# Performance work log

Hardware: AMD Instinct MI355X
Metric: run time of the kernel (lower is better)

## Reference

```python
import jax, jax.numpy as jnp
import numpy as np

B, T, D = 4, 2048, 2048
H, HD = 16, 128  # n_heads, head_dim; inner_dim = H*HD = 2048
SCALE = float(np.sqrt(HD))


def setup_inputs() -> dict:
    key = jax.random.key(0)
    kx, kq, kk, kv, ko = jax.random.split(key, 5)
    s = 0.02
    return {
        "x":  jax.random.normal(kx, (B, T, D), jnp.float32),
        "Wq": jax.random.normal(kq, (D, H * HD), jnp.float32) * s,
        "Wk": jax.random.normal(kk, (D, H * HD), jnp.float32) * s,
        "Wv": jax.random.normal(kv, (D, H * HD), jnp.float32) * s,
        "Wo": jax.random.normal(ko, (H * HD, D), jnp.float32) * s,
        "layer_idx": 0,
    }


def reference(x, Wq, Wk, Wv, Wo, layer_idx):
    # Cache starts empty and T <= max_cache_size, so cached_k/v == k/v and
    # T_cache == T; the sink/window mask reduces to a standard causal mask.
    b, t, _ = x.shape

    def split_heads(y):
        return y.reshape(b, t, H, HD).transpose(0, 2, 1, 3)  # (B,H,T,HD)

    q = split_heads(x @ Wq)
    k = split_heads(x @ Wk)
    v = split_heads(x @ Wv)

    scores = jnp.einsum('bhqd,bhkd->bhqk', q, k) / SCALE  # (B,H,T,T)
    q_idx = jnp.arange(t)
    k_idx = jnp.arange(t)
    causal = k_idx[None, :] <= q_idx[:, None]  # T_cache - T + q_idx == q_idx
    scores = jnp.where(causal[None, None], scores, -jnp.inf)
    w = jax.nn.softmax(scores, axis=-1)
    out = jnp.einsum('bhqk,bhkd->bhqd', w, v)
    out = out.transpose(0, 2, 1, 3).reshape(b, t, H * HD)
    return out @ Wo
```

## Files before the change

kernel.cpp:

```cpp
#include <hip/hip_runtime.h>
#include <hip/hip_bf16.h>
#include <stdint.h>

#define TT   2048
#define DD   2048
#define NH   16
#define NB   4
#define HDIM 128
#define MSZ  (NB * TT)
#define NQKV (3 * DD)
#define NT   32

typedef __attribute__((ext_vector_type(8))) __bf16 bf16x8;
typedef __attribute__((ext_vector_type(4))) float  f32x4;

typedef __attribute__((address_space(3))) void       lds_void;
typedef const __attribute__((address_space(1))) void g_void;

__device__ inline unsigned short f2bf(float f) {
  union { float f; unsigned u; } v; v.f = f;
  unsigned r = v.u + 0x7fffu + ((v.u >> 16) & 1u);
  return (unsigned short)(r >> 16);
}

__device__ inline void gload16(const void* g, void* l) {
  __builtin_amdgcn_global_load_lds((g_void*)g, (lds_void*)l, 16, 0, 0);
}

__device__ inline f32x4 mfma16(bf16x8 a, bf16x8 b, f32x4 c) {
  return __builtin_amdgcn_mfma_f32_16x16x32_bf16(a, b, c, 0, 0, 0);
}

__global__ __launch_bounds__(256) void cvtx(const float* __restrict__ x,
                                            unsigned short* __restrict__ xb) {
  const int n4 = MSZ * DD / 4;
  for (int i = blockIdx.x * blockDim.x + threadIdx.x; i < n4;
       i += gridDim.x * blockDim.x) {
    float4 v = ((const float4*)x)[i];
    uint2 u;
    u.x = (unsigned)f2bf(v.x) | ((unsigned)f2bf(v.y) << 16);
    u.y = (unsigned)f2bf(v.z) | ((unsigned)f2bf(v.w) << 16);
    *(uint2*)&xb[(size_t)i * 4] = u;
  }
}

__global__ __launch_bounds__(256) void transW(const float* __restrict__ Wq,
                                              const float* __restrict__ Wk,
                                              const float* __restrict__ Wv,
                                              const float* __restrict__ Wo,
                                              unsigned short* __restrict__ Wtq,
                                              unsigned short* __restrict__ Wto) {
  __shared__ float tl[32][33];
  const int z = blockIdx.z;
  const float* W = (z == 0) ? Wq : (z == 1) ? Wk : (z == 2) ? Wv : Wo;
  unsigned short* outp = (z < 3) ? (Wtq + (size_t)z * DD * DD) : Wto;
  const int c = threadIdx.x & 31, r8 = threadIdx.x >> 5;
  const int k0 = blockIdx.y * 32, n0 = blockIdx.x * 32;
#pragma unroll
  for (int i = 0; i < 4; ++i)
    tl[r8 + 8 * i][c] = W[(size_t)(k0 + r8 + 8 * i) * DD + n0 + c];
  __syncthreads();
#pragma unroll
  for (int i = 0; i < 4; ++i)
    outp[(size_t)(n0 + r8 + 8 * i) * DD + k0 + c] = f2bf(tl[c][r8 + 8 * i]);
}

template <int EPI>
__global__ __launch_bounds__(512, 2) void gemm8(
    const unsigned short* __restrict__ A, const unsigned short* __restrict__ Bt,
    unsigned short* __restrict__ Qb, unsigned short* __restrict__ Kb,
    unsigned short* __restrict__ Vt, float* __restrict__ Cf) {
  __shared__ __align__(16) unsigned short As[2][2][8192];
  __shared__ __align__(16) unsigned short Bs[2][2][8192];
  const int tid = threadIdx.x;
  const int lane = tid & 63;
  const int w = tid >> 6;
  const int wm = w >> 2, wn = w & 3;
  const int l15 = lane & 15, g = lane >> 4;
  const int m0 = blockIdx.y * 256, n0 = blockIdx.x * 256;

  const int u  = (tid * 16) ^ (((tid >> 5) & 1) << 5);
  const int sr = (u >> 6) & 127;
  const int sc = (u & 63) >> 1;
  const unsigned short* sA0 = A  + (size_t)(m0 + sr) * DD + sc;
  const unsigned short* sA1 = A  + (size_t)(m0 + 128 + sr) * DD + sc;
  const unsigned short* sB0 = Bt + (size_t)(n0 + sr) * DD + sc;
  const unsigned short* sB1 = Bt + (size_t)(n0 + 128 + sr) * DD + sc;

  const int pA = ((l15 * 64 + g * 16) ^ (((l15 >> 3) & 1) << 5)) >> 1;
  const int pB = (wn & 1) * 2048 + pA;

  f32x4 acc[8][4] = {};

#define STAGE(kt, hf)                                                         \
  do {                                                                        \
    if ((kt) < NT) {                                                          \
      const unsigned short* s_ = (hf) == 0 ? sA0 : (hf) == 1 ? sA1            \
                                 : (hf) == 2 ? sB0 : sB1;                     \
      s_ += (kt) * 64;                                                        \
      unsigned short* d_ = ((hf) < 2 ? &As[(kt) & 1][(hf) & 1][0]             \
                                     : &Bs[(kt) & 1][(hf) & 1][0]) + tid * 8; \
      gload16(s_, d_);                                                        \
      gload16(s_ + 32, d_ + 4096);                                            \
    }                                                                         \
  } while (0)

#define MFMAQ(q)                                                              \
  do {                                                                        \
    __builtin_amdgcn_s_setprio(1);                                            \
    _Pragma("unroll") for (int n2 = 0; n2 < 2; ++n2)                          \
    _Pragma("unroll") for (int m2 = 0; m2 < 4; ++m2)                          \
    _Pragma("unroll") for (int kk = 0; kk < 2; ++kk)                          \
      acc[((q) & 1) * 4 + m2][((q) >> 1) * 2 + n2] =                          \
          mfma16(af[((q) & 1) * 4 + m2][kk], bq[((q) >> 1) * 2 + n2][kk],     \
                 acc[((q) & 1) * 4 + m2][((q) >> 1) * 2 + n2]);               \
    __builtin_amdgcn_s_setprio(0);                                            \
  } while (0)

#define TILE(t, buf)                                                          \
  do {                                                                        \
    const unsigned short* Ab = &As[buf][wm][0];                               \
    const unsigned short* Bb = &Bs[buf][wn >> 1][0];                          \
    bf16x8 af[8][2], bq[4][2];                                                \
    _Pragma("unroll") for (int m = 0; m < 8; ++m) {                           \
      af[m][0] = *(const bf16x8*)&Ab[pA + m * 512];                           \
      af[m][1] = *(const bf16x8*)&Ab[pA + m * 512 + 4096];                    \
    }                                                                         \
    _Pragma("unroll") for (int n = 0; n < 4; ++n) {                           \
      bq[n][0] = *(const bf16x8*)&Bb[pB + n * 512];                           \
      bq[n][1] = *(const bf16x8*)&Bb[pB + n * 512 + 4096];                    \
    }                                                                         \
    STAGE((t) + 1, 3);                                                        \
    __builtin_amdgcn_s_barrier();                                             \
    MFMAQ(0);                                                                 \
    asm volatile("s_waitcnt lgkmcnt(0)" ::: "memory");                        \
    __builtin_amdgcn_sched_barrier(0);                                        \
    __builtin_amdgcn_s_barrier();                                             \
    STAGE((t) + 2, 0);                                                        \
    __builtin_amdgcn_s_barrier();                                             \
    MFMAQ(1);                                                                 \
    __builtin_amdgcn_s_barrier();                                             \
    STAGE((t) + 2, 1);                                                        \
    __builtin_amdgcn_s_barrier();                                             \
    MFMAQ(2);                                                                 \
    __builtin_amdgcn_s_barrier();                                             \
    STAGE((t) + 2, 2);                                                        \
    __builtin_amdgcn_s_barrier();                                             \
    MFMAQ(3);                                                                 \
    asm volatile("s_waitcnt vmcnt(6)" ::: "memory");                          \
    __builtin_amdgcn_sched_barrier(0);                                        \
    __builtin_amdgcn_s_barrier();                                             \
  } while (0)

  STAGE(0, 0); STAGE(0, 1); STAGE(0, 2); STAGE(0, 3);
  STAGE(1, 0); STAGE(1, 1); STAGE(1, 2);
  asm volatile("s_waitcnt vmcnt(6)" ::: "memory");
  __builtin_amdgcn_sched_barrier(0);
  __builtin_amdgcn_s_barrier();

#pragma unroll 1
  for (int it = 0; it < NT / 2; ++it) {
    TILE(2 * it, 0);
    TILE(2 * it + 1, 1);
  }
#undef TILE
#undef MFMAQ
#undef STAGE

  const float RSCALE = 0.08838834764831845f;
#pragma unroll
  for (int m = 0; m < 8; ++m) {
#pragma unroll
    for (int n = 0; n < 4; ++n) {
      const int row0 = m0 + wm * 128 + m * 16 + 4 * g;
      const int col2 = wn * 64 + n * 16;
      const int col = n0 + col2 + l15;
      if (EPI == 1) {
#pragma unroll
        for (int r = 0; r < 4; ++r)
          Cf[(size_t)(row0 + r) * DD + col] = acc[m][n][r];
      } else {
        const int mat = n0 >> 11;
        const int h = ((n0 & 2047) + col2) >> 7;
        const int hd = (col2 & 127) + l15;
        if (mat == 0) {
#pragma unroll
          for (int r = 0; r < 4; ++r) {
            const int mm = row0 + r, b = mm >> 11, t = mm & 2047;
            Qb[((size_t)(b * NH + h) * TT + t) * HDIM + hd] =
                f2bf(acc[m][n][r] * RSCALE);
          }
        } else if (mat == 1) {
#pragma unroll
          for (int r = 0; r < 4; ++r) {
            const int mm = row0 + r, b = mm >> 11, t = mm & 2047;
            Kb[((size_t)(b * NH + h) * TT + t) * HDIM + hd] = f2bf(acc[m][n][r]);
          }
        } else {
          const int b = row0 >> 11, t = row0 & 2047;
          uint2 uu;
          uu.x = (unsigned)f2bf(acc[m][n][0]) | ((unsigned)f2bf(acc[m][n][1]) << 16);
          uu.y = (unsigned)f2bf(acc[m][n][2]) | ((unsigned)f2bf(acc[m][n][3]) << 16);
          *(uint2*)&Vt[((size_t)(b * NH + h) * HDIM + hd) * TT + t] = uu;
        }
      }
    }
  }
}

__global__ __launch_bounds__(256, 4) void attn(const unsigned short* __restrict__ Qb,
                                               const unsigned short* __restrict__ Kb,
                                               const unsigned short* __restrict__ Vt,
                                               unsigned short* __restrict__ O) {
  __shared__ __align__(16) unsigned short Ks[2][4096];
  __shared__ __align__(16) unsigned short Vs[2][4096];
  __shared__ __align__(16) unsigned short pl[4][16][40];

  const int bx = blockIdx.x;
  const int bh = blockIdx.y;
  const int tid = threadIdx.x;
  const int w = tid >> 6;
  const int lane = tid & 63;
  const int l15 = lane & 15, g = lane >> 4;

  const unsigned short* Qh = Qb + (size_t)bh * TT * HDIM;
  const unsigned short* Kh = Kb + (size_t)bh * TT * HDIM;
  const unsigned short* Vh = Vt + (size_t)bh * HDIM * TT;
  const int b = bh >> 4, h = bh & 15;

  const int kch = tid >> 5, krow = tid & 31;
  const int vc = tid >> 7, vrow = tid & 127;

  int buf = 0;
#pragma unroll 1
  for (int ph = 0; ph < 2; ++ph) {
    const int qt = ph ? bx : (31 - bx);
    const int q0 = qt * 64 + w * 16;
    const int nt = 2 * qt + 2;

    bf16x8 qf[4];
#pragma unroll
    for (int kc = 0; kc < 4; ++kc)
      qf[kc] = *(const bf16x8*)&Qh[(size_t)(q0 + l15) * HDIM + kc * 32 + g * 8];

    f32x4 o[8] = {};
    float mrow[4], lrow[4];
#pragma unroll
    for (int r = 0; r < 4; ++r) { mrow[r] = -1e30f; lrow[r] = 0.f; }

    {
      const int kv0 = 0;
      gload16(Kh + (size_t)(kv0 + krow) * HDIM + kch * 8,      &Ks[buf][(kch * 32 + krow) * 8]);
      gload16(Kh + (size_t)(kv0 + krow) * HDIM + (kch + 8) * 8,&Ks[buf][((kch + 8) * 32 + krow) * 8]);
      gload16(Vh + (size_t)vrow * TT + kv0 + vc * 8,           &Vs[buf][(vc * 128 + vrow) * 8]);
      gload16(Vh + (size_t)vrow * TT + kv0 + (vc + 2) * 8,     &Vs[buf][((vc + 2) * 128 + vrow) * 8]);
    }

#pragma unroll 1
    for (int t = 0; t < nt; ++t) {
      const int kv0 = t * 32;
      __syncthreads();
      if (t + 1 < nt) {
        const int kvn = kv0 + 32;
        gload16(Kh + (size_t)(kvn + krow) * HDIM + kch * 8,      &Ks[buf ^ 1][(kch * 32 + krow) * 8]);
        gload16(Kh + (size_t)(kvn + krow) * HDIM + (kch + 8) * 8,&Ks[buf ^ 1][((kch + 8) * 32 + krow) * 8]);
        gload16(Vh + (size_t)vrow * TT + kvn + vc * 8,           &Vs[buf ^ 1][(vc * 128 + vrow) * 8]);
        gload16(Vh + (size_t)vrow * TT + kvn + (vc + 2) * 8,     &Vs[buf ^ 1][((vc + 2) * 128 + vrow) * 8]);
      }

      if (kv0 <= q0 + 15) {
        f32x4 s0 = {}, s1 = {};
#pragma unroll
        for (int kc = 0; kc < 4; ++kc) {
          bf16x8 k0 = *(const bf16x8*)&Ks[buf][((kc * 4 + g) * 32 + l15) * 8];
          bf16x8 k1 = *(const bf16x8*)&Ks[buf][((kc * 4 + g) * 32 + 16 + l15) * 8];
          s0 = mfma16(qf[kc], k0, s0);
          s1 = mfma16(qf[kc], k1, s1);
        }
        float pmax[4];
#pragma unroll
        for (int r = 0; r < 4; ++r) {
          const int q = q0 + 4 * g + r;
          if (kv0 + l15 > q) s0[r] = -1e30f;
          if (kv0 + 16 + l15 > q) s1[r] = -1e30f;
          pmax[r] = fmaxf(s0[r], s1[r]);
        }
#pragma unroll
        for (int off = 1; off < 16; off <<= 1) {
#pragma unroll
          for (int r = 0; r < 4; ++r)
            pmax[r] = fmaxf(pmax[r], __shfl_xor(pmax[r], off, 64));
        }
        float al[4], rs[4];
#pragma unroll
        for (int r = 0; r < 4; ++r) {
          const float mn = fmaxf(mrow[r], pmax[r]);
          al[r] = __expf(mrow[r] - mn);
          mrow[r] = mn;
          s0[r] = __expf(s0[r] - mn);
          s1[r] = __expf(s1[r] - mn);
          rs[r] = s0[r] + s1[r];
        }
#pragma unroll
        for (int off = 1; off < 16; off <<= 1) {
#pragma unroll
          for (int r = 0; r < 4; ++r) rs[r] += __shfl_xor(rs[r], off, 64);
        }
#pragma unroll
        for (int r = 0; r < 4; ++r) lrow[r] = lrow[r] * al[r] + rs[r];
#pragma unroll
        for (int n8 = 0; n8 < 8; ++n8)
#pragma unroll
          for (int r = 0; r < 4; ++r) o[n8][r] *= al[r];

#pragma unroll
        for (int r = 0; r < 4; ++r) {
          pl[w][4 * g + r][l15] = f2bf(s0[r]);
          pl[w][4 * g + r][16 + l15] = f2bf(s1[r]);
        }
        bf16x8 pf = *(const bf16x8*)&pl[w][l15][g * 8];
#pragma unroll
        for (int n8 = 0; n8 < 8; ++n8) {
          bf16x8 vf = *(const bf16x8*)&Vs[buf][(g * 128 + n8 * 16 + l15) * 8];
          o[n8] = mfma16(pf, vf, o[n8]);
        }
      }
      __syncthreads();
      buf ^= 1;
    }

    float linv[4];
#pragma unroll
    for (int r = 0; r < 4; ++r) linv[r] = 1.0f / lrow[r];
#pragma unroll
    for (int n8 = 0; n8 < 8; ++n8) {
#pragma unroll
      for (int r = 0; r < 4; ++r) {
        const int q = q0 + 4 * g + r;
        O[((size_t)(b * TT + q)) * (NH * HDIM) + h * HDIM + n8 * 16 + l15] =
            f2bf(o[n8][r] * linv[r]);
      }
    }
  }
}

extern "C" void kernel_launch(void* const* d_in, const int* in_sizes, int n_in,
                              void* d_out, int out_size, void* d_ws, size_t ws_size,
                              hipStream_t stream) {
  const float* x  = (const float*)d_in[0];
  const float* Wq = (const float*)d_in[1];
  const float* Wk = (const float*)d_in[2];
  const float* Wv = (const float*)d_in[3];
  const float* Wo = (const float*)d_in[4];
  float* out = (float*)d_out;

  char* ws = (char*)d_ws;
  size_t off = 0;
  unsigned short* xb  = (unsigned short*)(ws + off); off += (size_t)MSZ * DD * 2;
  unsigned short* Wtq = (unsigned short*)(ws + off); off += (size_t)NQKV * DD * 2;
  unsigned short* Wto = (unsigned short*)(ws + off); off += (size_t)DD * DD * 2;
  unsigned short* Qb  = (unsigned short*)(ws + off); off += (size_t)MSZ * DD * 2;
  unsigned short* Kb  = (unsigned short*)(ws + off); off += (size_t)MSZ * DD * 2;
  unsigned short* Vt  = (unsigned short*)(ws + off); off += (size_t)MSZ * DD * 2;
  unsigned short* Ob  = xb;

  cvtx<<<2048, 256, 0, stream>>>(x, xb);
  transW<<<dim3(64, 64, 4), 256, 0, stream>>>(Wq, Wk, Wv, Wo, Wtq, Wto);
  gemm8<0><<<dim3(NQKV / 256, MSZ / 256), 512, 0, stream>>>(xb, Wtq, Qb, Kb, Vt, nullptr);
  attn<<<dim3(16, NB * NH), 256, 0, stream>>>(Qb, Kb, Vt, Ob);
  gemm8<1><<<dim3(DD / 256, MSZ / 256), 512, 0, stream>>>(Ob, Wto, nullptr, nullptr, nullptr, out);
}
```

Before: 627.1 us.

## Streamline attention softmax with exp2, DPP reductions, lazy rescale, MFMA row sums

Folds log2(e) into the Q scale so the softmax can use the hardware exp2. Row max is reduced with DPP row-rotate moves instead of shuffles, and the output and running sum are rescaled only when some row max grows by more than a threshold. The row sum now comes from an MFMA against a ones vector instead of a shuffle reduction, and bf16 conversion uses the native cast. The attention grid is flattened and remapped so neighbouring blocks share heads, which should help L2 locality. The lazy rescale and the bf16-rounded row sum carry some numerical risk.

Measured after the change: 574.8 us. 8.3% less time.

```diff
diff --git a/kernel.cpp b/kernel.cpp
--- a/kernel.cpp
+++ b/kernel.cpp
@@ -23,6 +23,10 @@
   return (unsigned short)(r >> 16);
 }
 
+__device__ inline unsigned short bfc(float f) {
+  return __builtin_bit_cast(unsigned short, (__bf16)f);
+}
+
 __device__ inline void gload16(const void* g, void* l) {
   __builtin_amdgcn_global_load_lds((g_void*)g, (lds_void*)l, 16, 0, 0);
 }
@@ -30,6 +34,13 @@
 __device__ inline f32x4 mfma16(bf16x8 a, bf16x8 b, f32x4 c) {
   return __builtin_amdgcn_mfma_f32_16x16x32_bf16(a, b, c, 0, 0, 0);
 }
+
+#define RORMAX(x, C)                                                        \
+  do {                                                                      \
+    int pi_ = __builtin_amdgcn_mov_dpp(__builtin_bit_cast(int, x), (C),     \
+                                       0xF, 0xF, true);                     \
+    x = fmaxf(x, __builtin_bit_cast(float, pi_));                           \
+  } while (0)
 
 __global__ __launch_bounds__(256) void cvtx(const float* __restrict__ x,
                                             unsigned short* __restrict__ xb) {
@@ -167,7 +178,7 @@
 #undef MFMAQ
 #undef STAGE
 
-  const float RSCALE = 0.08838834764831845f;
+  const float QSCALE = 0.1275174308f;
 #pragma unroll
   for (int m = 0; m < 8; ++m) {
 #pragma unroll
@@ -188,7 +199,7 @@
           for (int r = 0; r < 4; ++r) {
             const int mm = row0 + r, b = mm >> 11, t = mm & 2047;
             Qb[((size_t)(b * NH + h) * TT + t) * HDIM + hd] =
-                f2bf(acc[m][n][r] * RSCALE);
+                f2bf(acc[m][n][r] * QSCALE);
           }
         } else if (mat == 1) {
 #pragma unroll
@@ -216,8 +227,9 @@
   __shared__ __align__(16) unsigned short Vs[2][4096];
   __shared__ __align__(16) unsigned short pl[4][16][40];
 
-  const int bx = blockIdx.x;
-  const int bh = blockIdx.y;
+  const int bid = blockIdx.x;
+  const int bx = (bid >> 3) & 15;
+  const int bh = (bid & 7) + 8 * (bid >> 7);
   const int tid = threadIdx.x;
   const int w = tid >> 6;
   const int lane = tid & 63;
@@ -227,6 +239,10 @@
   const unsigned short* Kh = Kb + (size_t)bh * TT * HDIM;
   const unsigned short* Vh = Vt + (size_t)bh * HDIM * TT;
   const int b = bh >> 4, h = bh & 15;
+
+  bf16x8 ones;
+#pragma unroll
+  for (int i = 0; i < 8; ++i) ones[i] = (__bf16)1.0f;
 
   const int kch = tid >> 5, krow = tid & 31;
   const int vc = tid >> 7, vrow = tid & 127;
@@ -286,39 +302,45 @@
           pmax[r] = fmaxf(s0[r], s1[r]);
         }
 #pragma unroll
-        for (int off = 1; off < 16; off <<= 1) {
-#pragma unroll
-          for (int r = 0; r < 4; ++r)
-            pmax[r] = fmaxf(pmax[r], __shfl_xor(pmax[r], off, 64));
-        }
-        float al[4], rs[4];
-#pragma unroll
         for (int r = 0; r < 4; ++r) {
-          const float mn = fmaxf(mrow[r], pmax[r]);
-          al[r] = __expf(mrow[r] - mn);
-          mrow[r] = mn;
-          s0[r] = __expf(s0[r] - mn);
-          s1[r] = __expf(s1[r] - mn);
-          rs[r] = s0[r] + s1[r];
-        }
-#pragma unroll
-        for (int off = 1; off < 16; off <<= 1) {
-#pragma unroll
-          for (int r = 0; r < 4; ++r) rs[r] += __shfl_xor(rs[r], off, 64);
-        }
-#pragma unroll
-        for (int r = 0; r < 4; ++r) lrow[r] = lrow[r] * al[r] + rs[r];
-#pragma unroll
-        for (int n8 = 0; n8 < 8; ++n8)
-#pragma unroll
-          for (int r = 0; r < 4; ++r) o[n8][r] *= al[r];
-
+          RORMAX(pmax[r], 0x121);
+          RORMAX(pmax[r], 0x122);
+          RORMAX(pmax[r], 0x124);
+          RORMAX(pmax[r], 0x128);
+        }
+        int need = 0;
+#pragma unroll
+        for (int r = 0; r < 4; ++r) need |= (pmax[r] > mrow[r] + 12.0f);
+        if (__any(need)) {
+          float al[4];
+#pragma unroll
+          for (int r = 0; r < 4; ++r) {
+            const float mn = fmaxf(mrow[r], pmax[r]);
+            al[r] = __builtin_amdgcn_exp2f(mrow[r] - mn);
+            mrow[r] = mn;
+            lrow[r] *= al[r];
+          }
+#pragma unroll
+          for (int n8 = 0; n8 < 8; ++n8)
+#pragma unroll
+            for (int r = 0; r < 4; ++r) o[n8][r] *= al[r];
+        }
 #pragma unroll
         for (int r = 0; r < 4; ++r) {
-          pl[w][4 * g + r][l15] = f2bf(s0[r]);
-          pl[w][4 * g + r][16 + l15] = f2bf(s1[r]);
+          s0[r] = __builtin_amdgcn_exp2f(s0[r] - mrow[r]);
+          s1[r] = __builtin_amdgcn_exp2f(s1[r] - mrow[r]);
+        }
+
+#pragma unroll
+        for (int r = 0; r < 4; ++r) {
+          pl[w][4 * g + r][l15] = bfc(s0[r]);
+          pl[w][4 * g + r][16 + l15] = bfc(s1[r]);
         }
         bf16x8 pf = *(const bf16x8*)&pl[w][l15][g * 8];
+        f32x4 z = {};
+        f32x4 sm = mfma16(pf, ones, z);
+#pragma unroll
+        for (int r = 0; r < 4; ++r) lrow[r] += sm[r];
 #pragma unroll
         for (int n8 = 0; n8 < 8; ++n8) {
           bf16x8 vf = *(const bf16x8*)&Vs[buf][(g * 128 + n8 * 16 + l15) * 8];
@@ -367,6 +389,6 @@
   cvtx<<<2048, 256, 0, stream>>>(x, xb);
   transW<<<dim3(64, 64, 4), 256, 0, stream>>>(Wq, Wk, Wv, Wo, Wtq, Wto);
   gemm8<0><<<dim3(NQKV / 256, MSZ / 256), 512, 0, stream>>>(xb, Wtq, Qb, Kb, Vt, nullptr);
-  attn<<<dim3(16, NB * NH), 256, 0, stream>>>(Qb, Kb, Vt, Ob);
+  attn<<<1024, 256, 0, stream>>>(Qb, Kb, Vt, Ob);
   gemm8<1><<<dim3(DD / 256, MSZ / 256), 512, 0, stream>>>(Ob, Wto, nullptr, nullptr, nullptr, out);
 }
```
